# Kernel tuning notes

Measured on AMD Instinct MI355X. Metric: run time of the kernel, lower is better.

The kernel has to match this reference:

```python
import jax, jax.numpy as jnp
import numpy as np

N_FLUID = 16384
N_BND = 2048
SUPPORT = float(np.sqrt(16.0 / (np.pi * N_FLUID)))  # ~16 neighbors avg
NB = 8  # basis functions per axis (n = m = 8)
NM = NB * NB
LAYERS = [32, 64, 64, 2]
F_IN = 8
B_IN = 8


def _radius(queries, points, r):
    """numpy brute-force (chunked) radius search; rows = query idx, cols = point idx."""
    r2 = np.float32(r * r)
    pn = (points ** 2).sum(-1)
    qi_all, pj_all = [], []
    for s in range(0, queries.shape[0], 4096):
        q = queries[s:s + 4096]
        d2 = (q ** 2).sum(-1)[:, None] + pn[None, :] - 2.0 * (q @ points.T)
        qi, pj = np.nonzero(d2 < r2)
        qi_all.append(qi + s)
        pj_all.append(pj)
    return (np.concatenate(qi_all).astype(np.int32),
            np.concatenate(pj_all).astype(np.int32))


def setup_inputs() -> dict:
    rng = np.random.default_rng(0)
    fluid_pos = rng.random((N_FLUID, 2)).astype(np.float32)
    # boundary particles along the perimeter of the unit square
    t = np.linspace(0.0, 4.0, N_BND, endpoint=False).astype(np.float32)
    side = np.floor(t).astype(np.int64)
    frac = t - side
    bx = np.where(side == 0, frac, np.where(side == 1, 1.0, np.where(side == 2, 1.0 - frac, 0.0)))
    by = np.where(side == 0, 0.0, np.where(side == 1, frac, np.where(side == 2, 1.0, 1.0 - frac)))
    bnd_pos = np.stack([bx, by], -1).astype(np.float32)

    # fluid-fluid radius graph (centerIgnore: drop self edges)
    fi, fj = _radius(fluid_pos, fluid_pos, SUPPORT)
    keep = fi != fj
    f_tgt, f_src = fi[keep], fj[keep]
    # fluid(query) - boundary(source) radius graph
    b_tgt, b_src = _radius(fluid_pos, bnd_pos, SUPPORT)

    def conv_w(k, cin, cout):
        return (0.05 * rng.standard_normal((NM, cin, cout))).astype(np.float32)

    def lin_w(cin, cout):
        s = np.sqrt(6.0 / (cin + cout))
        return rng.uniform(-s, s, (cin, cout)).astype(np.float32)

    d = {
        'fluid_pos': jnp.asarray(fluid_pos),
        'bnd_pos': jnp.asarray(bnd_pos),
        'fluid_feat': jnp.asarray(rng.standard_normal((N_FLUID, F_IN)).astype(np.float32)),
        'bnd_feat': jnp.asarray(rng.standard_normal((N_BND, B_IN)).astype(np.float32)),
        'f_tgt': jnp.asarray(f_tgt), 'f_src': jnp.asarray(f_src),
        'b_tgt': jnp.asarray(b_tgt), 'b_src': jnp.asarray(b_src),
        # convs: c0 fluid->fluid (F_IN->32), c1 boundary->fluid (B_IN->32),
        #        c2 (96->64), c3 (64->64), c4 (64->2)
        'Wc0': jnp.asarray(conv_w(0, F_IN, 32)), 'bc0': jnp.zeros((32,), jnp.float32),
        'Wc1': jnp.asarray(conv_w(1, B_IN, 32)), 'bc1': jnp.zeros((32,), jnp.float32),
        'Wc2': jnp.asarray(conv_w(2, 96, 64)), 'bc2': jnp.zeros((64,), jnp.float32),
        'Wc3': jnp.asarray(conv_w(3, 64, 64)), 'bc3': jnp.zeros((64,), jnp.float32),
        'Wc4': jnp.asarray(conv_w(4, 64, 2)), 'bc4': jnp.zeros((2,), jnp.float32),
        # dense branch: l0 (F_IN->32), l1 (96->64), l2 (64->64), l3 (64->2)
        'Wl0': jnp.asarray(lin_w(F_IN, 32)), 'bl0': jnp.zeros((32,), jnp.float32),
        'Wl1': jnp.asarray(lin_w(96, 64)), 'bl1': jnp.zeros((64,), jnp.float32),
        'Wl2': jnp.asarray(lin_w(64, 64)), 'bl2': jnp.zeros((64,), jnp.float32),
        'Wl3': jnp.asarray(lin_w(64, 2)), 'bl3': jnp.zeros((2,), jnp.float32),
    }
    return d


def _hat(x, n):
    # linear 'hat' RBF basis on centers in [-1, 1]
    c = jnp.linspace(-1.0, 1.0, n, dtype=x.dtype)
    return jnp.maximum(0.0, 1.0 - jnp.abs(x[:, None] - c[None, :]) * ((n - 1) / 2.0))


def _polar(d):
    # polar coordinate mapping of normalized displacement d in [-1,1]^2
    r = jnp.sqrt(jnp.sum(d * d, -1) + 1e-12)
    theta = jnp.arctan2(d[:, 1], d[:, 0])
    return jnp.clip(jnp.stack([2.0 * r - 1.0, theta / jnp.pi], -1), -1.0, 1.0)


def _rbf_conv(x_src_nodes, src, tgt, disp, W, b, num_tgt):
    m = _polar(disp)                                   # [E,2]
    bx = _hat(m[:, 0], NB)                             # [E,n]
    by = _hat(m[:, 1], NB)                             # [E,m]
    basis = (bx[:, :, None] * by[:, None, :]).reshape(-1, NM)  # [E,nm]
    xs = x_src_nodes[src]                              # [E,cin]
    acc0 = jnp.zeros((xs.shape[0], W.shape[-1]), xs.dtype)

    def body(acc, wb):
        Wk, bk = wb
        return acc + bk[:, None] * (xs @ Wk), None

    msg, _ = jax.lax.scan(body, acc0, (W, basis.T))    # sum_k basis_k * (xs @ W_k)
    return jax.ops.segment_sum(msg, tgt, num_segments=num_tgt) + b


def reference(fluid_pos, bnd_pos, fluid_feat, bnd_feat, f_tgt, f_src, b_tgt, b_src,
              Wc0, bc0, Wc1, bc1, Wc2, bc2, Wc3, bc3, Wc4, bc4,
              Wl0, bl0, Wl1, bl1, Wl2, bl2, Wl3, bl3):
    N = fluid_feat.shape[0]
    fdisp = jnp.clip(-(fluid_pos[f_src] - fluid_pos[f_tgt]) / SUPPORT, -1.0, 1.0)
    bdisp = jnp.clip((bnd_pos[b_src] - fluid_pos[b_tgt]) / SUPPORT, -1.0, 1.0)

    lin = fluid_feat @ Wl0 + bl0
    fconv = _rbf_conv(fluid_feat, f_src, f_tgt, fdisp, Wc0, bc0, N)
    bconv = _rbf_conv(bnd_feat, b_src, b_tgt, bdisp, Wc1, bc1, N)
    ans = jnp.concatenate([lin, fconv, bconv], axis=-1)  # [N, 96]

    blocks = [(Wc2, bc2, Wl1, bl1, False), (Wc3, bc3, Wl2, bl2, True), (Wc4, bc4, Wl3, bl3, False)]
    for Wc, bc, Wl, bl, residual in blocks:
        a = jax.nn.relu(ans)
        c = _rbf_conv(a, f_src, f_tgt, fdisp, Wc, bc, N)
        dns = a @ Wl + bl
        ans = c + dns + ans if residual else c + dns
    return ans / 128.0
```

## Files before the change

### kernel.cpp

```cpp
#include <hip/hip_runtime.h>
#include <math.h>
#include <stdint.h>

#define NFL   16384
#define NCC   55
#define PADQ  128

struct EdgeData { int src; int ixiy; float fx; float fy; };

typedef _Float16 half8 __attribute__((ext_vector_type(8)));
typedef __attribute__((ext_vector_type(4))) float f32x4;

__device__ __forceinline__ float frelu(float x){ return x > 0.f ? x : 0.f; }
__device__ __forceinline__ unsigned short f2bf(float f){
    unsigned int u = __float_as_uint(f);
    unsigned int r = (u + 0x7FFFu + ((u >> 16) & 1u)) >> 16;
    return (unsigned short)r;
}

__global__ void prep_edges_k(const float* __restrict__ qpos,
                             const float* __restrict__ ppos,
                             const int* __restrict__ tgt,
                             const int* __restrict__ src,
                             int nE, float support, float sgn,
                             EdgeData* __restrict__ out)
{
    int e = blockIdx.x * blockDim.x + threadIdx.x;
    if (e >= nE) return;
    int t = tgt[e], s = src[e];
    float dx = sgn * (ppos[2*s]   - qpos[2*t])   / support;
    float dy = sgn * (ppos[2*s+1] - qpos[2*t+1]) / support;
    dx = fminf(1.f, fmaxf(-1.f, dx));
    dy = fminf(1.f, fmaxf(-1.f, dy));
    float r  = sqrtf(dx*dx + dy*dy + 1e-12f);
    float th = atan2f(dy, dx);
    float m0 = fminf(1.f, fmaxf(-1.f, 2.f*r - 1.f));
    float m1 = fminf(1.f, fmaxf(-1.f, th * 0.3183098861837907f));
    float u = (m0 + 1.f) * 3.5f;
    float v = (m1 + 1.f) * 3.5f;
    int ix = (int)u; if (ix > 6) ix = 6;
    int iy = (int)v; if (iy > 6) iy = 6;
    EdgeData ed;
    ed.src  = s;
    ed.ixiy = ix*8 + iy;
    ed.fx   = u - (float)ix;
    ed.fy   = v - (float)iy;
    out[e] = ed;
}

__global__ void rowptr_k(const int* __restrict__ tgt, int nE, int* __restrict__ rowptr)
{
    int t = blockIdx.x * blockDim.x + threadIdx.x;
    if (t > NFL) return;
    if (t == NFL){ rowptr[NFL] = nE; return; }
    int lo = 0, hi = nE;
    while (lo < hi){ int mid = (lo + hi) >> 1; if (tgt[mid] < t) lo = mid + 1; else hi = mid; }
    rowptr[t] = lo;
}

__global__ void zero64_k(int* __restrict__ a){ if (threadIdx.x < 64) a[threadIdx.x] = 0; }

__global__ void hist_k(const EdgeData* __restrict__ ed, int nE, int* __restrict__ cnt)
{
    __shared__ int lc[64];
    int tid = threadIdx.x;
    if (tid < 64) lc[tid] = 0;
    __syncthreads();
    int e = blockIdx.x * blockDim.x + tid;
    if (e < nE) atomicAdd(&lc[ed[e].ixiy], 1);
    __syncthreads();
    if (tid < 64 && lc[tid] > 0) atomicAdd(&cnt[tid], lc[tid]);
}

__global__ void scan_pad_k(const int* __restrict__ cnt, int* __restrict__ cellOff,
                           int* __restrict__ gcursor)
{
    if (threadIdx.x < 64) gcursor[threadIdx.x] = 0;
    if (threadIdx.x == 0){
        int s = 0;
        for (int k = 0; k < NCC; ++k){
            cellOff[k] = s;
            s += ((cnt[k] + PADQ - 1) / PADQ) * PADQ;
        }
        cellOff[NCC] = s;
    }
}

__global__ void fill_entries_k(int4* __restrict__ entries, int n)
{
    int i = blockIdx.x * blockDim.x + threadIdx.x;
    if (i < n) entries[i] = make_int4(0, -1, 0, 0);
}

__global__ void scatter_k(const EdgeData* __restrict__ ed, int nE,
                          const int* __restrict__ cellOff,
                          int* __restrict__ gcursor,
                          int4* __restrict__ entries)
{
    __shared__ int lc[64], base[64];
    int tid = threadIdx.x;
    if (tid < 64) lc[tid] = 0;
    __syncthreads();
    int e = blockIdx.x * blockDim.x + tid;
    bool ok = e < nE;
    EdgeData d; int k = 0, r = 0;
    if (ok){ d = ed[e]; k = d.ixiy; r = atomicAdd(&lc[k], 1); }
    __syncthreads();
    if (tid < 64 && lc[tid] > 0) base[tid] = atomicAdd(&gcursor[tid], lc[tid]);
    __syncthreads();
    if (ok){
        int slot = cellOff[k] + base[k] + r;
        entries[slot] = make_int4(d.src, e, __float_as_int(d.fx), __float_as_int(d.fy));
    }
}

__global__ void wcvt_k(const float* __restrict__ in, unsigned short* __restrict__ out, int n)
{
    int i = blockIdx.x * blockDim.x + threadIdx.x;
    if (i < n) out[i] = f2bf(in[i]);
}

template<int CIN>
__global__ __launch_bounds__(256)
void wtr_k(const float* __restrict__ Wsrc, _Float16* __restrict__ wt)
{
    constexpr int COUT = 64;
    __shared__ _Float16 T[COUT][CIN + 2];
    int cell = blockIdx.x;
    const float* s = Wsrc + (size_t)cell * CIN * COUT;
    for (int i = threadIdx.x; i < CIN*COUT; i += 256){
        int k = i / COUT, c = i - k*COUT;
        T[c][k] = (_Float16)s[i];
    }
    __syncthreads();
    _Float16* d = wt + (size_t)cell * COUT * CIN;
    for (int i = threadIdx.x; i < CIN*COUT; i += 256){
        int c = i / CIN, k = i - c*CIN;
        d[i] = T[c][k];
    }
}

template<int CIN>
__global__ __launch_bounds__(256)
void conv_mfma_k(const _Float16* __restrict__ xh,
                 const int4* __restrict__ entries,
                 const int* __restrict__ cellOff,
                 const _Float16* __restrict__ wt,
                 _Float16* __restrict__ msg)
{
    constexpr int COUT = 64;
    constexpr int XROW = CIN*2 + 16;
    constexpr int C16  = CIN*2/16;

    __shared__ unsigned char XL[64 * XROW];
    __shared__ float BW[4][64];
    __shared__ int   SRC[64];
    __shared__ int   EID[64];

    int total = cellOff[NCC];
    int p0 = blockIdx.x * 64;
    if (p0 >= total) return;
    int tid = threadIdx.x;

    int lo_ = 0, hi_ = NCC;
    while (hi_ - lo_ > 1){ int mid = (lo_ + hi_) >> 1; if (cellOff[mid] <= p0) lo_ = mid; else hi_ = mid; }
    const int cell = lo_;
    const int kc[4] = { cell, cell+1, cell+8, cell+9 };

    if (tid < 64){
        int4 en = entries[p0 + tid];
        bool ok = en.y >= 0;
        float fx = __int_as_float(en.z), fy = __int_as_float(en.w);
        BW[0][tid] = ok ? (1.f-fx)*(1.f-fy) : 0.f;
        BW[1][tid] = ok ? (1.f-fx)*fy       : 0.f;
        BW[2][tid] = ok ? fx*(1.f-fy)       : 0.f;
        BW[3][tid] = ok ? fx*fy             : 0.f;
        SRC[tid] = en.x;
        EID[tid] = en.y;
    }
    __syncthreads();
    for (int i = tid; i < 64*C16; i += 256){
        int e = i / C16, c = i - e*C16;
        const uint4* sp = (const uint4*)(xh + (size_t)SRC[e]*CIN) + c;
        *(uint4*)(&XL[e*XROW + 16*c]) = *sp;
    }
    __syncthreads();

    const int lane = tid & 63, wv = tid >> 6;
    const int lr = lane & 15, lg = lane >> 4;
    const int cb = wv * 16;

    const _Float16* wbase = wt + (size_t)(cb + lr) * CIN + lg * 8;

    f32x4 acc[4][4];
#pragma unroll
    for (int cr = 0; cr < 4; ++cr)
#pragma unroll
        for (int ae = 0; ae < 4; ++ae)
            acc[cr][ae] = (f32x4)0.f;

#pragma unroll
    for (int k0 = 0; k0 < CIN; k0 += 32){
        half8 b[4], a[4];
#pragma unroll
        for (int cr = 0; cr < 4; ++cr)
            b[cr] = *(const half8*)(wbase + (size_t)kc[cr]*(COUT*CIN) + k0);
#pragma unroll
        for (int ae = 0; ae < 4; ++ae)
            a[ae] = *(const half8*)(XL + (16*ae + lr)*XROW + k0*2 + lg*16);
#pragma unroll
        for (int cr = 0; cr < 4; ++cr)
#pragma unroll
            for (int ae = 0; ae < 4; ++ae)
                acc[cr][ae] = __builtin_amdgcn_mfma_f32_16x16x32_f16(a[ae], b[cr], acc[cr][ae], 0, 0, 0);
    }

#pragma unroll
    for (int ae = 0; ae < 4; ++ae){
#pragma unroll
        for (int r = 0; r < 4; ++r){
            int E = 16*ae + lg*4 + r;
            int eid = EID[E];
            if (eid >= 0){
                float v = BW[0][E]*acc[0][ae][r] + BW[1][E]*acc[1][ae][r]
                        + BW[2][E]*acc[2][ae][r] + BW[3][E]*acc[3][ae][r];
                msg[(size_t)eid*COUT + cb + lr] = (_Float16)v;
            }
        }
    }
}

template<int CIN, int COUT, int TILE_E, bool RELU>
__global__ __launch_bounds__(128)
void conv_cell_k(const float* __restrict__ x,
                 const int4* __restrict__ entries,
                 const int* __restrict__ cellOff,
                 const unsigned short* __restrict__ Wbf,
                 _Float16* __restrict__ msg)
{
    constexpr int TEP = TILE_E + 4;
    constexpr int EG  = TILE_E / 4;
    constexpr int CG  = COUT / 8;
    static_assert(EG * CG == 128, "tile/thread mismatch");
    constexpr int C4  = CIN / 4;

    __shared__ float XT[CIN][TEP];
    __shared__ unsigned short WLc[4][CIN][COUT];
    __shared__ int4 EN[TILE_E];

    int total = cellOff[NCC];
    int p0 = blockIdx.x * TILE_E;
    if (p0 >= total) return;
    int tid = threadIdx.x;

    int lo = 0, hi = NCC;
    while (hi - lo > 1){ int mid = (lo + hi) >> 1; if (cellOff[mid] <= p0) lo = mid; else hi = mid; }
    const int cell = lo;

    for (int i = tid; i < TILE_E; i += 128) EN[i] = entries[p0 + i];

    const int kc[4] = { cell, cell + 1, cell + 8, cell + 9 };
#pragma unroll
    for (int c = 0; c < 4; ++c){
        const uint4* s = (const uint4*)(Wbf + (size_t)kc[c] * (CIN * COUT));
        uint4* dlds = (uint4*)(&WLc[c][0][0]);
        for (int i = tid; i < CIN * COUT / 8; i += 128) dlds[i] = s[i];
    }
    __syncthreads();

    for (int i = tid; i < TILE_E * C4; i += 128){
        int e  = i / C4;
        int c4 = i - e * C4;
        int4 en = EN[e];
        float4 v = make_float4(0.f, 0.f, 0.f, 0.f);
        if (en.y >= 0){
            v = *(const float4*)(x + (size_t)en.x * CIN + 4 * c4);
            if (RELU){ v.x = frelu(v.x); v.y = frelu(v.y); v.z = frelu(v.z); v.w = frelu(v.w); }
        }
        XT[4*c4+0][e] = v.x;
        XT[4*c4+1][e] = v.y;
        XT[4*c4+2][e] = v.z;
        XT[4*c4+3][e] = v.w;
    }
    __syncthreads();

    const int egrp = tid % EG;
    const int cgrp = tid / EG;
    const int e0 = egrp * 4;

    float fx[4], fy[4];
    int eid[4];
#pragma unroll
    for (int j = 0; j < 4; ++j){
        int4 en = EN[e0 + j];
        fx[j] = __int_as_float(en.z);
        fy[j] = __int_as_float(en.w);
        eid[j] = en.y;
    }

    float accT[4][8];
#pragma unroll
    for (int j = 0; j < 4; ++j)
#pragma unroll
        for (int c = 0; c < 8; ++c) accT[j][c] = 0.f;

#pragma unroll
    for (int cr = 0; cr < 4; ++cr){
        float accC[4][8];
#pragma unroll
        for (int j = 0; j < 4; ++j)
#pragma unroll
            for (int c = 0; c < 8; ++c) accC[j][c] = 0.f;

#pragma unroll
        for (int ci = 0; ci < CIN; ++ci){
            float4 xv = *(const float4*)&XT[ci][e0];
            uint4 wp = *(const uint4*)&WLc[cr][ci][cgrp * 8];
            float wf0 = __uint_as_float(wp.x << 16);
            float wf1 = __uint_as_float(wp.x & 0xFFFF0000u);
            float wf2 = __uint_as_float(wp.y << 16);
            float wf3 = __uint_as_float(wp.y & 0xFFFF0000u);
            float wf4 = __uint_as_float(wp.z << 16);
            float wf5 = __uint_as_float(wp.z & 0xFFFF0000u);
            float wf6 = __uint_as_float(wp.w << 16);
            float wf7 = __uint_as_float(wp.w & 0xFFFF0000u);
            const float xe[4] = { xv.x, xv.y, xv.z, xv.w };
#pragma unroll
            for (int j = 0; j < 4; ++j){
                accC[j][0] += xe[j] * wf0;
                accC[j][1] += xe[j] * wf1;
                accC[j][2] += xe[j] * wf2;
                accC[j][3] += xe[j] * wf3;
                accC[j][4] += xe[j] * wf4;
                accC[j][5] += xe[j] * wf5;
                accC[j][6] += xe[j] * wf6;
                accC[j][7] += xe[j] * wf7;
            }
        }
#pragma unroll
        for (int j = 0; j < 4; ++j){
            float wc = (cr == 0) ? (1.f - fx[j]) * (1.f - fy[j]) :
                       (cr == 1) ? (1.f - fx[j]) * fy[j] :
                       (cr == 2) ? fx[j] * (1.f - fy[j]) :
                                   fx[j] * fy[j];
#pragma unroll
            for (int c = 0; c < 8; ++c) accT[j][c] += wc * accC[j][c];
        }
    }

#pragma unroll
    for (int j = 0; j < 4; ++j){
        if (eid[j] < 0) continue;
        half8 hv;
#pragma unroll
        for (int c = 0; c < 8; ++c) hv[c] = (_Float16)accT[j][c];
        *(half8*)(msg + (size_t)eid[j] * COUT + cgrp * 8) = hv;
    }
}

__global__ __launch_bounds__(128)
void conv2_msg_k(const _Float16* __restrict__ xh,
                 const int4* __restrict__ entries,
                 const int* __restrict__ cellOff,
                 const float* __restrict__ Wc,
                 float* __restrict__ msg2)
{
    __shared__ float WLf[4][64][2];
    int total = cellOff[NCC];
    int p0 = blockIdx.x * 128;
    if (p0 >= total) return;
    int tid = threadIdx.x;

    int lo = 0, hi = NCC;
    while (hi - lo > 1){ int mid = (lo + hi) >> 1; if (cellOff[mid] <= p0) lo = mid; else hi = mid; }
    const int cell = lo;
    const int kc[4] = { cell, cell + 1, cell + 8, cell + 9 };
#pragma unroll
    for (int c = 0; c < 4; ++c)
        ((float*)&WLf[c][0][0])[tid] = Wc[(size_t)kc[c] * 128 + tid];
    __syncthreads();

    int4 en = entries[p0 + tid];
    if (en.y < 0) return;
    float fx = __int_as_float(en.z), fy = __int_as_float(en.w);
    const _Float16* xp = xh + (size_t)en.x * 64;

    float a[4][2] = {{0.f,0.f},{0.f,0.f},{0.f,0.f},{0.f,0.f}};
#pragma unroll
    for (int ci = 0; ci < 64; ci += 8){
        half8 v = *(const half8*)(xp + ci);
#pragma unroll
        for (int j = 0; j < 8; ++j){
            float xe = (float)v[j];
#pragma unroll
            for (int cr = 0; cr < 4; ++cr){
                a[cr][0] += xe * WLf[cr][ci+j][0];
                a[cr][1] += xe * WLf[cr][ci+j][1];
            }
        }
    }
    float w0 = (1.f-fx)*(1.f-fy), w1 = (1.f-fx)*fy, w2 = fx*(1.f-fy), w3 = fx*fy;
    float m0 = w0*a[0][0] + w1*a[1][0] + w2*a[2][0] + w3*a[3][0];
    float m1 = w0*a[0][1] + w1*a[1][1] + w2*a[2][1] + w3*a[3][1];
    *(float2*)(msg2 + (size_t)en.y * 2) = make_float2(m0, m1);
}

__global__ __launch_bounds__(256)
void final_combine_k(const float* __restrict__ y2,
                     const float* __restrict__ Wl3, const float* __restrict__ bl3,
                     const float* __restrict__ bc4,
                     const float* __restrict__ msg2,
                     const int* __restrict__ rowptr,
                     float* __restrict__ out)
{
    __shared__ float WS[128];
    int tid = threadIdx.x;
    if (tid < 128) WS[tid] = Wl3[tid];
    __syncthreads();

    int t = blockIdx.x * blockDim.x + tid;
    if (t >= NFL) return;
    int eb = rowptr[t], ee = rowptr[t+1];

    float a0 = bc4[0] + bl3[0];
    float a1 = bc4[1] + bl3[1];
    const float* pr = y2 + (size_t)t * 64;
#pragma unroll 4
    for (int ci = 0; ci < 64; ci += 4){
        float4 v = *(const float4*)(pr + ci);
        float xe[4] = { frelu(v.x), frelu(v.y), frelu(v.z), frelu(v.w) };
#pragma unroll
        for (int j = 0; j < 4; ++j){
            a0 += xe[j] * WS[(ci+j)*2];
            a1 += xe[j] * WS[(ci+j)*2 + 1];
        }
    }
    for (int e = eb; e < ee; ++e){
        float2 m = *(const float2*)(msg2 + (size_t)e * 2);
        a0 += m.x; a1 += m.y;
    }
    out[(size_t)t*2]     = a0 * (1.0f/128.0f);
    out[(size_t)t*2 + 1] = a1 * (1.0f/128.0f);
}

__global__ __launch_bounds__(256)
void combine0_k(const float* __restrict__ feat,
                const float* __restrict__ bnd_feat,
                const float* __restrict__ Wl0, const float* __restrict__ bl0,
                const float* __restrict__ bc0,
                const float* __restrict__ Wc1, const float* __restrict__ bc1,
                const EdgeData* __restrict__ edB,
                const int* __restrict__ rowptrB,
                const _Float16* __restrict__ msg,
                const int* __restrict__ rowptrF,
                float* __restrict__ ansA,
                _Float16* __restrict__ xbA)
{
    int t = blockIdx.x * (blockDim.x >> 6) + (threadIdx.x >> 6);
    if (t >= NFL) return;
    int lane = threadIdx.x & 63;

    if (lane < 32){
        float a = bl0[lane];
#pragma unroll
        for (int ci = 0; ci < 8; ++ci)
            a += feat[t*8 + ci] * Wl0[ci*32 + lane];
        ansA[(size_t)t*96 + lane] = a;
        xbA[(size_t)t*96 + lane]  = (_Float16)frelu(a);

        float b = bc1[lane];
        int eb = rowptrB[t], ee = rowptrB[t+1];
        for (int e = eb; e < ee; ++e){
            EdgeData d = edB[e];
            const float* xp = bnd_feat + (size_t)d.src * 8;
            const float* wp = Wc1 + (size_t)d.ixiy * 256 + lane;
            float t00 = 0.f, t01 = 0.f, t10 = 0.f, t11 = 0.f;
#pragma unroll
            for (int ci = 0; ci < 8; ++ci){
                float xv = xp[ci];
                t00 += xv * wp[ci*32];
                t01 += xv * wp[ci*32 + 256];
                t10 += xv * wp[ci*32 + 2048];
                t11 += xv * wp[ci*32 + 2304];
            }
            float wx1 = d.fx, wy1 = d.fy;
            float wx0 = 1.f - wx1, wy0 = 1.f - wy1;
            b += (wx0*wy0)*t00 + (wx0*wy1)*t01 + (wx1*wy0)*t10 + (wx1*wy1)*t11;
        }
        ansA[(size_t)t*96 + 64 + lane] = b;
        xbA[(size_t)t*96 + 64 + lane]  = (_Float16)frelu(b);
    } else {
        int c = lane - 32;
        float a = bc0[c];
        int eb = rowptrF[t], ee = rowptrF[t+1];
        for (int e = eb; e < ee; ++e)
            a += (float)msg[(size_t)e*32 + c];
        ansA[(size_t)t*96 + 32 + c] = a;
        xbA[(size_t)t*96 + 32 + c]  = (_Float16)frelu(a);
    }
}

template<int CIN, bool RESID, bool WRITE_XB>
__global__ __launch_bounds__(256)
void combine12_k(const float* __restrict__ prev,
                 const float* __restrict__ Wl, const float* __restrict__ bl,
                 const float* __restrict__ bc,
                 const _Float16* __restrict__ msg,
                 const int* __restrict__ rowptr,
                 float* __restrict__ y,
                 _Float16* __restrict__ xbnext)
{
    int t = blockIdx.x * (blockDim.x >> 6) + (threadIdx.x >> 6);
    if (t >= NFL) return;
    int lane = threadIdx.x & 63;
    int eb = rowptr[t], ee = rowptr[t+1];

    const float* pr = prev + (size_t)t * CIN;
    float acc = bc[lane] + bl[lane];
#pragma unroll 8
    for (int ci = 0; ci < CIN; ++ci)
        acc += frelu(pr[ci]) * Wl[ci*64 + lane];
    if (RESID) acc += pr[lane];

    for (int e = eb; e < ee; ++e)
        acc += (float)msg[(size_t)e*64 + lane];
    y[(size_t)t*64 + lane] = acc;

    if (WRITE_XB)
        xbnext[(size_t)t*64 + lane] = (_Float16)frelu(acc);
}

extern "C" void kernel_launch(void* const* d_in, const int* in_sizes, int n_in,
                              void* d_out, int out_size, void* d_ws, size_t ws_size,
                              hipStream_t stream)
{
    const float* fluid_pos  = (const float*)d_in[0];
    const float* bnd_pos    = (const float*)d_in[1];
    const float* fluid_feat = (const float*)d_in[2];
    const float* bnd_feat   = (const float*)d_in[3];
    const int*   f_tgt      = (const int*)  d_in[4];
    const int*   f_src      = (const int*)  d_in[5];
    const int*   b_tgt      = (const int*)  d_in[6];
    const int*   b_src      = (const int*)  d_in[7];
    const float* Wc0 = (const float*)d_in[8];  const float* bc0 = (const float*)d_in[9];
    const float* Wc1 = (const float*)d_in[10]; const float* bc1 = (const float*)d_in[11];
    const float* Wc2 = (const float*)d_in[12]; const float* bc2 = (const float*)d_in[13];
    const float* Wc3 = (const float*)d_in[14]; const float* bc3 = (const float*)d_in[15];
    const float* Wc4 = (const float*)d_in[16]; const float* bc4 = (const float*)d_in[17];
    const float* Wl0 = (const float*)d_in[18]; const float* bl0 = (const float*)d_in[19];
    const float* Wl1 = (const float*)d_in[20]; const float* bl1 = (const float*)d_in[21];
    const float* Wl2 = (const float*)d_in[22]; const float* bl2 = (const float*)d_in[23];
    const float* Wl3 = (const float*)d_in[24]; const float* bl3 = (const float*)d_in[25];

    int nEf = in_sizes[4];
    int nEb = in_sizes[6];
    int entPadMax = nEf + NCC * PADQ;
    float support = (float)sqrt(16.0 / (M_PI * 16384.0));

    char* w = (char*)d_ws;
    auto alloc = [&](size_t bytes){ char* r = w; w += (bytes + 255) & ~(size_t)255; return r; };
    EdgeData* edF      = (EdgeData*)alloc((size_t)nEf * sizeof(EdgeData));
    EdgeData* edB      = (EdgeData*)alloc((size_t)nEb * sizeof(EdgeData));
    int*      cnt      = (int*)     alloc(64 * sizeof(int));
    int*      cellOff  = (int*)     alloc(64 * sizeof(int));
    int*      gcursor  = (int*)     alloc(64 * sizeof(int));
    int*      rowptrF  = (int*)     alloc((NFL+1) * sizeof(int));
    int*      rowptrB  = (int*)     alloc((NFL+1) * sizeof(int));
    int4*     entries  = (int4*)    alloc((size_t)entPadMax * sizeof(int4));
    unsigned short* wb0 = (unsigned short*)alloc((size_t)64*8*32 * 2);
    _Float16* wt2      = (_Float16*)alloc((size_t)64*64*96 * 2);
    _Float16* wt3      = (_Float16*)alloc((size_t)64*64*64 * 2);
    _Float16* xbA      = (_Float16*)alloc((size_t)NFL*96 * 2);
    _Float16* xb1      = (_Float16*)alloc((size_t)NFL*64 * 2);
    _Float16* xb2      = (_Float16*)alloc((size_t)NFL*64 * 2);
    float*    ansA     = (float*)   alloc((size_t)NFL * 96 * sizeof(float));
    float*    y1       = (float*)   alloc((size_t)NFL * 64 * sizeof(float));
    float*    y2       = (float*)   alloc((size_t)NFL * 64 * sizeof(float));
    _Float16* msg      = (_Float16*)alloc((size_t)nEf * 64 * 2);
    float*    msg2     = (float*)   alloc((size_t)nEf * 2 * sizeof(float));

    prep_edges_k<<<(nEf+255)/256, 256, 0, stream>>>(fluid_pos, fluid_pos, f_tgt, f_src, nEf, support, -1.f, edF);
    prep_edges_k<<<(nEb+255)/256, 256, 0, stream>>>(fluid_pos, bnd_pos,   b_tgt, b_src, nEb, support,  1.f, edB);
    rowptr_k<<<(NFL+1+255)/256, 256, 0, stream>>>(f_tgt, nEf, rowptrF);
    rowptr_k<<<(NFL+1+255)/256, 256, 0, stream>>>(b_tgt, nEb, rowptrB);
    zero64_k<<<1, 64, 0, stream>>>(cnt);
    hist_k<<<(nEf+255)/256, 256, 0, stream>>>(edF, nEf, cnt);
    scan_pad_k<<<1, 64, 0, stream>>>(cnt, cellOff, gcursor);
    fill_entries_k<<<(entPadMax+255)/256, 256, 0, stream>>>(entries, entPadMax);
    scatter_k<<<(nEf+255)/256, 256, 0, stream>>>(edF, nEf, cellOff, gcursor, entries);

    wcvt_k<<<(64*8*32 +255)/256, 256, 0, stream>>>(Wc0, wb0, 64*8*32);
    wtr_k<96><<<64, 256, 0, stream>>>(Wc2, wt2);
    wtr_k<64><<<64, 256, 0, stream>>>(Wc3, wt3);

    int gridM   = (entPadMax + 63)  / 64;
    int grid128 = (entPadMax + 127) / 128;
    dim3 tgrid(NFL/4);

    conv_cell_k<8,32,128,false><<<grid128, 128, 0, stream>>>(fluid_feat, entries, cellOff, wb0, msg);
    combine0_k<<<tgrid, 256, 0, stream>>>(fluid_feat, bnd_feat, Wl0, bl0, bc0,
                                          Wc1, bc1, edB, rowptrB,
                                          msg, rowptrF, ansA, xbA);

    conv_mfma_k<96><<<gridM, 256, 0, stream>>>(xbA, entries, cellOff, wt2, msg);
    combine12_k<96,false,true><<<tgrid, 256, 0, stream>>>(ansA, Wl1, bl1, bc2, msg, rowptrF, y1, xb1);

    conv_mfma_k<64><<<gridM, 256, 0, stream>>>(xb1, entries, cellOff, wt3, msg);
    combine12_k<64,true,true><<<tgrid, 256, 0, stream>>>(y1, Wl2, bl2, bc3, msg, rowptrF, y2, xb2);

    conv2_msg_k<<<grid128, 128, 0, stream>>>(xb2, entries, cellOff, Wc4, msg2);
    final_combine_k<<<(NFL+255)/256, 256, 0, stream>>>(y2, Wl3, bl3, bc4, msg2, rowptrF, (float*)d_out);
}
```

Measured before the change: 293.1 us.

## Fuse setup kernels, pad-only fill, two chunks per MFMA block, fp16 relu input

Merges edge prep, histogram and both rowptr searches into one multi-role setup kernel, and merges the three weight-conversion kernels into one. The scan kernel now writes only the padding slots instead of a full-array fill pass, which cuts launch count and memory traffic. The MFMA conv kernel handles two 64-entry chunks per block, halving the grid and reusing the cell lookup. The dense paths of the combine kernels read the already-relu'd fp16 activations instead of fp32 values followed by relu, which adds fp16 rounding into the dense term.

```diff
diff --git a/kernel.cpp b/kernel.cpp
--- a/kernel.cpp
+++ b/kernel.cpp
@@ -18,16 +18,9 @@
     return (unsigned short)r;
 }
 
-__global__ void prep_edges_k(const float* __restrict__ qpos,
-                             const float* __restrict__ ppos,
-                             const int* __restrict__ tgt,
-                             const int* __restrict__ src,
-                             int nE, float support, float sgn,
-                             EdgeData* __restrict__ out)
-{
-    int e = blockIdx.x * blockDim.x + threadIdx.x;
-    if (e >= nE) return;
-    int t = tgt[e], s = src[e];
+__device__ __forceinline__ EdgeData make_edge(const float* qpos, const float* ppos,
+                                              int t, int s, float support, float sgn)
+{
     float dx = sgn * (ppos[2*s]   - qpos[2*t])   / support;
     float dy = sgn * (ppos[2*s+1] - qpos[2*t+1]) / support;
     dx = fminf(1.f, fmaxf(-1.f, dx));
@@ -45,51 +38,76 @@
     ed.ixiy = ix*8 + iy;
     ed.fx   = u - (float)ix;
     ed.fy   = v - (float)iy;
-    out[e] = ed;
-}
-
-__global__ void rowptr_k(const int* __restrict__ tgt, int nE, int* __restrict__ rowptr)
-{
-    int t = blockIdx.x * blockDim.x + threadIdx.x;
-    if (t > NFL) return;
-    if (t == NFL){ rowptr[NFL] = nE; return; }
-    int lo = 0, hi = nE;
-    while (lo < hi){ int mid = (lo + hi) >> 1; if (tgt[mid] < t) lo = mid + 1; else hi = mid; }
-    rowptr[t] = lo;
-}
-
-__global__ void zero64_k(int* __restrict__ a){ if (threadIdx.x < 64) a[threadIdx.x] = 0; }
-
-__global__ void hist_k(const EdgeData* __restrict__ ed, int nE, int* __restrict__ cnt)
-{
-    __shared__ int lc[64];
+    return ed;
+}
+
+__global__ __launch_bounds__(256)
+void setup_k(const float* __restrict__ fluid_pos, const float* __restrict__ bnd_pos,
+             const int* __restrict__ f_tgt, const int* __restrict__ f_src, int nEf,
+             const int* __restrict__ b_tgt, const int* __restrict__ b_src, int nEb,
+             float support,
+             EdgeData* __restrict__ edF, EdgeData* __restrict__ edB,
+             int* __restrict__ cnt,
+             int* __restrict__ rowptrF, int* __restrict__ rowptrB,
+             int nA, int nB, int nC)
+{
+    int b = blockIdx.x, tid = threadIdx.x;
+    if (b < nA){
+        __shared__ int lc[64];
+        if (tid < 64) lc[tid] = 0;
+        __syncthreads();
+        int e = b*256 + tid;
+        if (e < nEf){
+            EdgeData d = make_edge(fluid_pos, fluid_pos, f_tgt[e], f_src[e], support, -1.f);
+            edF[e] = d;
+            atomicAdd(&lc[d.ixiy], 1);
+        }
+        __syncthreads();
+        if (tid < 64 && lc[tid] > 0) atomicAdd(&cnt[tid], lc[tid]);
+    } else if (b < nA + nB){
+        int e = (b - nA)*256 + tid;
+        if (e < nEb)
+            edB[e] = make_edge(fluid_pos, bnd_pos, b_tgt[e], b_src[e], support, 1.f);
+    } else if (b < nA + nB + nC){
+        int t = (b - nA - nB)*256 + tid;
+        if (t > NFL) return;
+        if (t == NFL){ rowptrF[NFL] = nEf; return; }
+        int lo = 0, hi = nEf;
+        while (lo < hi){ int mid = (lo + hi) >> 1; if (f_tgt[mid] < t) lo = mid + 1; else hi = mid; }
+        rowptrF[t] = lo;
+    } else {
+        int t = (b - nA - nB - nC)*256 + tid;
+        if (t > NFL) return;
+        if (t == NFL){ rowptrB[NFL] = nEb; return; }
+        int lo = 0, hi = nEb;
+        while (lo < hi){ int mid = (lo + hi) >> 1; if (b_tgt[mid] < t) lo = mid + 1; else hi = mid; }
+        rowptrB[t] = lo;
+    }
+}
+
+__global__ __launch_bounds__(256)
+void scan_pad_k(const int* __restrict__ cnt, int* __restrict__ cellOff,
+                int* __restrict__ gcursor, int4* __restrict__ entries)
+{
+    __shared__ int offS[NCC+1], cntS[NCC];
     int tid = threadIdx.x;
-    if (tid < 64) lc[tid] = 0;
-    __syncthreads();
-    int e = blockIdx.x * blockDim.x + tid;
-    if (e < nE) atomicAdd(&lc[ed[e].ixiy], 1);
-    __syncthreads();
-    if (tid < 64 && lc[tid] > 0) atomicAdd(&cnt[tid], lc[tid]);
-}
-
-__global__ void scan_pad_k(const int* __restrict__ cnt, int* __restrict__ cellOff,
-                           int* __restrict__ gcursor)
-{
-    if (threadIdx.x < 64) gcursor[threadIdx.x] = 0;
-    if (threadIdx.x == 0){
+    if (tid < 64) gcursor[tid] = 0;
+    if (tid == 0){
         int s = 0;
         for (int k = 0; k < NCC; ++k){
-            cellOff[k] = s;
-            s += ((cnt[k] + PADQ - 1) / PADQ) * PADQ;
-        }
-        cellOff[NCC] = s;
-    }
-}
-
-__global__ void fill_entries_k(int4* __restrict__ entries, int n)
-{
-    int i = blockIdx.x * blockDim.x + threadIdx.x;
-    if (i < n) entries[i] = make_int4(0, -1, 0, 0);
+            offS[k] = s; int c = cnt[k]; cntS[k] = c;
+            s += ((c + PADQ - 1) / PADQ) * PADQ;
+        }
+        offS[NCC] = s;
+        for (int k = 0; k <= NCC; ++k) cellOff[k] = offS[k];
+    }
+    __syncthreads();
+    for (int k = 0; k < NCC; ++k){
+        int base = offS[k] + cntS[k];
+        int pads = (offS[k+1] - offS[k]) - cntS[k];
+        for (int i = tid; i < pads; i += 256)
+            entries[base + i] = make_int4(0, -1, 0, 0);
+    }
 }
 
 __global__ void scatter_k(const EdgeData* __restrict__ ed, int nE,
@@ -114,29 +132,29 @@
     }
 }
 
-__global__ void wcvt_k(const float* __restrict__ in, unsigned short* __restrict__ out, int n)
-{
-    int i = blockIdx.x * blockDim.x + threadIdx.x;
-    if (i < n) out[i] = f2bf(in[i]);
-}
-
-template<int CIN>
 __global__ __launch_bounds__(256)
-void wtr_k(const float* __restrict__ Wsrc, _Float16* __restrict__ wt)
-{
-    constexpr int COUT = 64;
-    __shared__ _Float16 T[COUT][CIN + 2];
-    int cell = blockIdx.x;
-    const float* s = Wsrc + (size_t)cell * CIN * COUT;
-    for (int i = threadIdx.x; i < CIN*COUT; i += 256){
-        int k = i / COUT, c = i - k*COUT;
-        T[c][k] = (_Float16)s[i];
-    }
-    __syncthreads();
-    _Float16* d = wt + (size_t)cell * COUT * CIN;
-    for (int i = threadIdx.x; i < CIN*COUT; i += 256){
-        int c = i / CIN, k = i - c*CIN;
-        d[i] = T[c][k];
+void wprep_k(const float* __restrict__ Wc2, const float* __restrict__ Wc3,
+             const float* __restrict__ Wc0,
+             _Float16* __restrict__ wt2, _Float16* __restrict__ wt3,
+             unsigned short* __restrict__ wb0)
+{
+    __shared__ _Float16 T[64][98];
+    int b = blockIdx.x, tid = threadIdx.x;
+    if (b < 64){
+        const float* s = Wc2 + (size_t)b * 96 * 64;
+        for (int i = tid; i < 96*64; i += 256){ int k = i/64, c = i - k*64; T[c][k] = (_Float16)s[i]; }
+        __syncthreads();
+        _Float16* d = wt2 + (size_t)b * 64 * 96;
+        for (int i = tid; i < 96*64; i += 256){ int c = i/96, k = i - c*96; d[i] = T[c][k]; }
+    } else if (b < 128){
+        int cell = b - 64;
+        const float* s = Wc3 + (size_t)cell * 64 * 64;
+        for (int i = tid; i < 64*64; i += 256){ int k = i/64, c = i - k*64; T[c][k] = (_Float16)s[i]; }
+        __syncthreads();
+        _Float16* d = wt3 + (size_t)cell * 64 * 64;
+        for (int i = tid; i < 64*64; i += 256){ int c = i/64, k = i - c*64; d[i] = T[c][k]; }
+    } else {
+        for (int i = tid; i < 64*8*32; i += 256) wb0[i] = f2bf(Wc0[i]);
     }
 }
 
@@ -158,75 +176,79 @@
     __shared__ int   EID[64];
 
     int total = cellOff[NCC];
-    int p0 = blockIdx.x * 64;
-    if (p0 >= total) return;
+    int pb = blockIdx.x * 128;
+    if (pb >= total) return;
     int tid = threadIdx.x;
 
     int lo_ = 0, hi_ = NCC;
-    while (hi_ - lo_ > 1){ int mid = (lo_ + hi_) >> 1; if (cellOff[mid] <= p0) lo_ = mid; else hi_ = mid; }
+    while (hi_ - lo_ > 1){ int mid = (lo_ + hi_) >> 1; if (cellOff[mid] <= pb) lo_ = mid; else hi_ = mid; }
     const int cell = lo_;
     const int kc[4] = { cell, cell+1, cell+8, cell+9 };
-
-    if (tid < 64){
-        int4 en = entries[p0 + tid];
-        bool ok = en.y >= 0;
-        float fx = __int_as_float(en.z), fy = __int_as_float(en.w);
-        BW[0][tid] = ok ? (1.f-fx)*(1.f-fy) : 0.f;
-        BW[1][tid] = ok ? (1.f-fx)*fy       : 0.f;
-        BW[2][tid] = ok ? fx*(1.f-fy)       : 0.f;
-        BW[3][tid] = ok ? fx*fy             : 0.f;
-        SRC[tid] = en.x;
-        EID[tid] = en.y;
-    }
-    __syncthreads();
-    for (int i = tid; i < 64*C16; i += 256){
-        int e = i / C16, c = i - e*C16;
-        const uint4* sp = (const uint4*)(xh + (size_t)SRC[e]*CIN) + c;
-        *(uint4*)(&XL[e*XROW + 16*c]) = *sp;
-    }
-    __syncthreads();
 
     const int lane = tid & 63, wv = tid >> 6;
     const int lr = lane & 15, lg = lane >> 4;
     const int cb = wv * 16;
-
     const _Float16* wbase = wt + (size_t)(cb + lr) * CIN + lg * 8;
 
-    f32x4 acc[4][4];
-#pragma unroll
-    for (int cr = 0; cr < 4; ++cr)
-#pragma unroll
-        for (int ae = 0; ae < 4; ++ae)
-            acc[cr][ae] = (f32x4)0.f;
-
-#pragma unroll
-    for (int k0 = 0; k0 < CIN; k0 += 32){
-        half8 b[4], a[4];
+    for (int ch = 0; ch < 2; ++ch){
+        int p0 = pb + ch * 64;
+
+        if (tid < 64){
+            int4 en = entries[p0 + tid];
+            bool ok = en.y >= 0;
+            float fx = __int_as_float(en.z), fy = __int_as_float(en.w);
+            BW[0][tid] = ok ? (1.f-fx)*(1.f-fy) : 0.f;
+            BW[1][tid] = ok ? (1.f-fx)*fy       : 0.f;
+            BW[2][tid] = ok ? fx*(1.f-fy)       : 0.f;
+            BW[3][tid] = ok ? fx*fy             : 0.f;
+            SRC[tid] = en.x;
+            EID[tid] = en.y;
+        }
+        __syncthreads();
+        for (int i = tid; i < 64*C16; i += 256){
+            int e = i / C16, c = i - e*C16;
+            const uint4* sp = (const uint4*)(xh + (size_t)SRC[e]*CIN) + c;
+            *(uint4*)(&XL[e*XROW + 16*c]) = *sp;
+        }
+        __syncthreads();
+
+        f32x4 acc[4][4];
 #pragma unroll
         for (int cr = 0; cr < 4; ++cr)
-            b[cr] = *(const half8*)(wbase + (size_t)kc[cr]*(COUT*CIN) + k0);
-#pragma unroll
-        for (int ae = 0; ae < 4; ++ae)
-            a[ae] = *(const half8*)(XL + (16*ae + lr)*XROW + k0*2 + lg*16);
-#pragma unroll
-        for (int cr = 0; cr < 4; ++cr)
 #pragma unroll
             for (int ae = 0; ae < 4; ++ae)
-                acc[cr][ae] = __builtin_amdgcn_mfma_f32_16x16x32_f16(a[ae], b[cr], acc[cr][ae], 0, 0, 0);
-    }
-
-#pragma unroll
-    for (int ae = 0; ae < 4; ++ae){
-#pragma unroll
-        for (int r = 0; r < 4; ++r){
-            int E = 16*ae + lg*4 + r;
-            int eid = EID[E];
-            if (eid >= 0){
-                float v = BW[0][E]*acc[0][ae][r] + BW[1][E]*acc[1][ae][r]
-                        + BW[2][E]*acc[2][ae][r] + BW[3][E]*acc[3][ae][r];
-                msg[(size_t)eid*COUT + cb + lr] = (_Float16)v;
+                acc[cr][ae] = (f32x4)0.f;
+
+#pragma unroll
+        for (int k0 = 0; k0 < CIN; k0 += 32){
+            half8 b[4], a[4];
+#pragma unroll
+            for (int cr = 0; cr < 4; ++cr)
+                b[cr] = *(const half8*)(wbase + (size_t)kc[cr]*(COUT*CIN) + k0);
+#pragma unroll
+            for (int ae = 0; ae < 4; ++ae)
+                a[ae] = *(const half8*)(XL + (16*ae + lr)*XROW + k0*2 + lg*16);
+#pragma unroll
+            for (int cr = 0; cr < 4; ++cr)
+#pragma unroll
+                for (int ae = 0; ae < 4; ++ae)
+                    acc[cr][ae] = __builtin_amdgcn_mfma_f32_16x16x32_f16(a[ae], b[cr], acc[cr][ae], 0, 0, 0);
+        }
+
+#pragma unroll
+        for (int ae = 0; ae < 4; ++ae){
+#pragma unroll
+            for (int r = 0; r < 4; ++r){
+                int E = 16*ae + lg*4 + r;
+                int eid = EID[E];
+                if (eid >= 0){
+                    float v = BW[0][E]*acc[0][ae][r] + BW[1][E]*acc[1][ae][r]
+                            + BW[2][E]*acc[2][ae][r] + BW[3][E]*acc[3][ae][r];
+                    msg[(size_t)eid*COUT + cb + lr] = (_Float16)v;
+                }
             }
         }
+        __syncthreads();
     }
 }
 
@@ -502,7 +524,8 @@
 
 template<int CIN, bool RESID, bool WRITE_XB>
 __global__ __launch_bounds__(256)
-void combine12_k(const float* __restrict__ prev,
+void combine12_k(const float* __restrict__ yprev,
+                 const _Float16* __restrict__ xprev,
                  const float* __restrict__ Wl, const float* __restrict__ bl,
                  const float* __restrict__ bc,
                  const _Float16* __restrict__ msg,
@@ -515,12 +538,12 @@
     int lane = threadIdx.x & 63;
     int eb = rowptr[t], ee = rowptr[t+1];
 
-    const float* pr = prev + (size_t)t * CIN;
+    const _Float16* pr = xprev + (size_t)t * CIN;
     float acc = bc[lane] + bl[lane];
 #pragma unroll 8
     for (int ci = 0; ci < CIN; ++ci)
-        acc += frelu(pr[ci]) * Wl[ci*64 + lane];
-    if (RESID) acc += pr[lane];
+        acc += (float)pr[ci] * Wl[ci*64 + lane];
+    if (RESID) acc += yprev[(size_t)t*64 + lane];
 
     for (int e = eb; e < ee; ++e)
         acc += (float)msg[(size_t)e*64 + lane];
@@ -579,35 +602,31 @@
     _Float16* msg      = (_Float16*)alloc((size_t)nEf * 64 * 2);
     float*    msg2     = (float*)   alloc((size_t)nEf * 2 * sizeof(float));
 
-    prep_edges_k<<<(nEf+255)/256, 256, 0, stream>>>(fluid_pos, fluid_pos, f_tgt, f_src, nEf, support, -1.f, edF);
-    prep_edges_k<<<(nEb+255)/256, 256, 0, stream>>>(fluid_pos, bnd_pos,   b_tgt, b_src, nEb, support,  1.f, edB);
-    rowptr_k<<<(NFL+1+255)/256, 256, 0, stream>>>(f_tgt, nEf, rowptrF);
-    rowptr_k<<<(NFL+1+255)/256, 256, 0, stream>>>(b_tgt, nEb, rowptrB);
-    zero64_k<<<1, 64, 0, stream>>>(cnt);
-    hist_k<<<(nEf+255)/256, 256, 0, stream>>>(edF, nEf, cnt);
-    scan_pad_k<<<1, 64, 0, stream>>>(cnt, cellOff, gcursor);
-    fill_entries_k<<<(entPadMax+255)/256, 256, 0, stream>>>(entries, entPadMax);
-    scatter_k<<<(nEf+255)/256, 256, 0, stream>>>(edF, nEf, cellOff, gcursor, entries);
-
-    wcvt_k<<<(64*8*32 +255)/256, 256, 0, stream>>>(Wc0, wb0, 64*8*32);
-    wtr_k<96><<<64, 256, 0, stream>>>(Wc2, wt2);
-    wtr_k<64><<<64, 256, 0, stream>>>(Wc3, wt3);
-
-    int gridM   = (entPadMax + 63)  / 64;
-    int grid128 = (entPadMax + 127) / 128;
+    hipMemsetAsync(cnt, 0, 64 * sizeof(int), stream);
+    int nA = (nEf + 255)/256, nB = (nEb + 255)/256, nC = (NFL + 256)/256;
+    setup_k<<<nA + nB + 2*nC, 256, 0, stream>>>(fluid_pos, bnd_pos,
+                                                f_tgt, f_src, nEf,
+                                                b_tgt, b_src, nEb, support,
+                                                edF, edB, cnt, rowptrF, rowptrB,
+                                                nA, nB, nC);
+    scan_pad_k<<<1, 256, 0, stream>>>(cnt, cellOff, gcursor, entries);
+    scatter_k<<<nA, 256, 0, stream>>>(edF, nEf, cellOff, gcursor, entries);
+    wprep_k<<<129, 256, 0, stream>>>(Wc2, Wc3, Wc0, wt2, wt3, wb0);
+
+    int gridM   = (entPadMax + 127) / 128;
     dim3 tgrid(NFL/4);
 
-    conv_cell_k<8,32,128,false><<<grid128, 128, 0, stream>>>(fluid_feat, entries, cellOff, wb0, msg);
+    conv_cell_k<8,32,128,false><<<gridM, 128, 0, stream>>>(fluid_feat, entries, cellOff, wb0, msg);
     combine0_k<<<tgrid, 256, 0, stream>>>(fluid_feat, bnd_feat, Wl0, bl0, bc0,
                                           Wc1, bc1, edB, rowptrB,
                                           msg, rowptrF, ansA, xbA);
 
     conv_mfma_k<96><<<gridM, 256, 0, stream>>>(xbA, entries, cellOff, wt2, msg);
-    combine12_k<96,false,true><<<tgrid, 256, 0, stream>>>(ansA, Wl1, bl1, bc2, msg, rowptrF, y1, xb1);
+    combine12_k<96,false,true><<<tgrid, 256, 0, stream>>>(nullptr, xbA, Wl1, bl1, bc2, msg, rowptrF, y1, xb1);
 
     conv_mfma_k<64><<<gridM, 256, 0, stream>>>(xb1, entries, cellOff, wt3, msg);
-    combine12_k<64,true,true><<<tgrid, 256, 0, stream>>>(y1, Wl2, bl2, bc3, msg, rowptrF, y2, xb2);
-
-    conv2_msg_k<<<grid128, 128, 0, stream>>>(xb2, entries, cellOff, Wc4, msg2);
+    combine12_k<64,true,true><<<tgrid, 256, 0, stream>>>(y1, xb1, Wl2, bl2, bc3, msg, rowptrF, y2, xb2);
+
+    conv2_msg_k<<<gridM, 128, 0, stream>>>(xb2, entries, cellOff, Wc4, msg2);
     final_combine_k<<<(NFL+255)/256, 256, 0, stream>>>(y2, Wl3, bl3, bc4, msg2, rowptrF, (float*)d_out);
 }
```

Measured after the change: 283.0 us. -3.4%, faster.
